# Kernel optimization log

Hardware: AMD Instinct MI355X
Metric: run time of the kernel (lower is better)

The kernel has to match this reference:

```python
import math
import jax, jax.numpy as jnp
import numpy as np

B = 64
INPUT_SIZE = 10080
PATCH = 18
S = INPUT_SIZE // PATCH  # 560 patches
E = 96                    # embed_dim
H = 12                    # num_heads
D = 96                    # head_dim == embed_dim (PAT quirk)
F = 256                   # ff_dim
L = 2                     # num_layers
EPS = 1e-5


def _sinusoidal_pe(seq_len, embed_dim):
    pos = jnp.arange(seq_len, dtype=jnp.float32)[:, None]
    div = jnp.exp(jnp.arange(0, embed_dim, 2, dtype=jnp.float32) * (-math.log(10000.0) / embed_dim))
    pe = jnp.zeros((seq_len, embed_dim), dtype=jnp.float32)
    pe = pe.at[:, 0::2].set(jnp.sin(pos * div))
    pe = pe.at[:, 1::2].set(jnp.cos(pos * div))
    return pe


def _layernorm(x, g, b):
    mu = jnp.mean(x, axis=-1, keepdims=True)
    var = jnp.var(x, axis=-1, keepdims=True)
    return (x - mu) * jax.lax.rsqrt(var + EPS) * g + b


def setup_inputs() -> dict:
    key = jax.random.key(0)
    ks = jax.random.split(key, 12)
    sd = 0.02
    inp = {
        "x": jax.random.normal(ks[0], (B, INPUT_SIZE), dtype=jnp.float32),
        "patch_W": jax.random.normal(ks[1], (PATCH, E), dtype=jnp.float32) * sd,
        "patch_b": jnp.zeros((E,), jnp.float32),
        "Wq": jax.random.normal(ks[2], (L, H, E, D), dtype=jnp.float32) * sd,
        "bq": jnp.zeros((L, H, D), jnp.float32),
        "Wk": jax.random.normal(ks[3], (L, H, E, D), dtype=jnp.float32) * sd,
        "bk": jnp.zeros((L, H, D), jnp.float32),
        "Wv": jax.random.normal(ks[4], (L, H, E, D), dtype=jnp.float32) * sd,
        "bv": jnp.zeros((L, H, D), jnp.float32),
        "Wo": jax.random.normal(ks[5], (L, H * D, E), dtype=jnp.float32) * sd,
        "bo": jnp.zeros((L, E), jnp.float32),
        "ff1_W": jax.random.normal(ks[6], (L, E, F), dtype=jnp.float32) * sd,
        "ff1_b": jnp.zeros((L, F), jnp.float32),
        "ff2_W": jax.random.normal(ks[7], (L, F, E), dtype=jnp.float32) * sd,
        "ff2_b": jnp.zeros((L, E), jnp.float32),
        "n1_g": jnp.ones((L, E), jnp.float32),
        "n1_b": jnp.zeros((L, E), jnp.float32),
        "n2_g": jnp.ones((L, E), jnp.float32),
        "n2_b": jnp.zeros((L, E), jnp.float32),
    }
    return inp


def reference(x, patch_W, patch_b, Wq, bq, Wk, bk, Wv, bv, Wo, bo,
              ff1_W, ff1_b, ff2_W, ff2_b, n1_g, n1_b, n2_g, n2_b):
    scale = 1.0 / math.sqrt(D)
    # patch embedding: [B, S, PATCH] -> [B, S, E]
    h = x.reshape(B, S, PATCH) @ patch_W + patch_b
    h = h + _sinusoidal_pe(S, E)[None]
    for l in range(L):
        # all heads at once (original loops over heads; same math)
        q = jnp.einsum('bse,hed->bhsd', h, Wq[l]) + bq[l][None, :, None, :]
        k = jnp.einsum('bse,hed->bhsd', h, Wk[l]) + bk[l][None, :, None, :]
        v = jnp.einsum('bse,hed->bhsd', h, Wv[l]) + bv[l][None, :, None, :]
        scores = jnp.einsum('bhsd,bhtd->bhst', q, k) * scale
        attn = jax.nn.softmax(scores, axis=-1)
        heads = jnp.einsum('bhst,bhtd->bhsd', attn, v)
        concat = heads.transpose(0, 2, 1, 3).reshape(B, S, H * D)
        attn_out = concat @ Wo[l] + bo[l]
        h = _layernorm(h + attn_out, n1_g[l], n1_b[l])
        ff = jax.nn.relu(h @ ff1_W[l] + ff1_b[l]) @ ff2_W[l] + ff2_b[l]
        h = _layernorm(h + ff, n2_g[l], n2_b[l])
    return h
```

## Files before the change

### kernel.cpp

```cpp
#include <hip/hip_runtime.h>
#include <hip/hip_bf16.h>
#include <math.h>

#define BATCH 64
#define CHUNK 32
#define INPUT_SIZE 10080
#define PATCH 18
#define SEQ 560
#define EMB 96
#define NHEAD 12
#define HDIM 96
#define FFDIM 256
#define NLAYER 2
#define TOK (BATCH * SEQ)
#define EPSV 1e-5f
#define SCALE 0.10206207261596577f
#define SCALE_L2E 0.14724443805513492f

typedef __attribute__((ext_vector_type(8))) short bf16x8;
typedef __attribute__((ext_vector_type(4))) short bf16x4;
typedef __attribute__((ext_vector_type(4))) float f32x4;
typedef __attribute__((ext_vector_type(2))) unsigned int u32x2;

static __device__ __forceinline__ short f2bf(float x) {
  union { __hip_bfloat16 b; short s; } u;
  u.b = __float2bfloat16(x);
  return u.s;
}

static __device__ __forceinline__ unsigned int pack2bf(float lo, float hi) {
  unsigned int a = (unsigned short)f2bf(lo);
  unsigned int b = (unsigned short)f2bf(hi);
  return a | (b << 16);
}

static __device__ __forceinline__ float exp2_fast(float x) {
  float r;
  asm("v_exp_f32 %0, %1" : "=v"(r) : "v"(x));
  return r;
}

__global__ __launch_bounds__(256) void allprep_kernel(
    const float* __restrict__ Wq, const float* __restrict__ Wk,
    const float* __restrict__ Wv, const float* __restrict__ Wo,
    const float* __restrict__ ff1_W, const float* __restrict__ ff2_W,
    __hip_bfloat16* __restrict__ wqT, __hip_bfloat16* __restrict__ wkvT,
    __hip_bfloat16* __restrict__ woT, __hip_bfloat16* __restrict__ ff1WT,
    __hip_bfloat16* __restrict__ ff2WT) {
  int bx = blockIdx.x;
  if (bx < 72) {
    int hh = bx % NHEAD, mat = (bx / NHEAD) % 3, l = bx / 36;
    const float* src = (mat == 0 ? Wq : (mat == 1 ? Wk : Wv)) +
                       ((size_t)l * NHEAD + hh) * EMB * HDIM;
    __shared__ float t[HDIM * 97];
    for (int i = threadIdx.x; i < EMB * HDIM; i += 256) {
      int e = i / HDIM, d = i % HDIM;
      t[d * 97 + e] = src[i];
    }
    __syncthreads();
    __hip_bfloat16* dst;
    if (mat == 0)
      dst = wqT + ((size_t)l * NHEAD + hh) * HDIM * EMB;
    else
      dst = wkvT + ((size_t)l * 2 * NHEAD * HDIM + (mat - 1) * NHEAD * HDIM +
                    hh * HDIM) * EMB;
    for (int j = threadIdx.x; j < HDIM * EMB; j += 256) {
      int d = j / EMB, e = j % EMB;
      dst[j] = __float2bfloat16(t[d * 97 + e]);
    }
  } else if (bx < 74) {
    int l = bx - 72;
    const float* src = Wo + (size_t)l * NHEAD * HDIM * EMB;
    __hip_bfloat16* dst = woT + (size_t)l * EMB * NHEAD * HDIM;
    for (int i = threadIdx.x; i < EMB * NHEAD * HDIM; i += 256) {
      int e = i / (NHEAD * HDIM), j = i % (NHEAD * HDIM);
      dst[i] = __float2bfloat16(src[(size_t)j * EMB + e]);
    }
  } else {
    int idx = bx - 74;
    int mat = idx % 2, l = idx / 2;
    if (mat == 0) {
      const float* src = ff1_W + (size_t)l * EMB * FFDIM;
      __hip_bfloat16* dst = ff1WT + (size_t)l * FFDIM * EMB;
      for (int i = threadIdx.x; i < FFDIM * EMB; i += 256) {
        int f = i / EMB, e = i % EMB;
        dst[i] = __float2bfloat16(src[(size_t)e * FFDIM + f]);
      }
    } else {
      const float* src = ff2_W + (size_t)l * FFDIM * EMB;
      __hip_bfloat16* dst = ff2WT + (size_t)l * EMB * FFDIM;
      for (int i = threadIdx.x; i < EMB * FFDIM; i += 256) {
        int e = i / FFDIM, f = i % FFDIM;
        dst[i] = __float2bfloat16(src[(size_t)f * EMB + e]);
      }
    }
  }
}

__global__ void patch_pe_kernel(const float* __restrict__ x,
                                const float* __restrict__ W,
                                const float* __restrict__ bias,
                                float* __restrict__ h,
                                __hip_bfloat16* __restrict__ hbf) {
  int gid = blockIdx.x * blockDim.x + threadIdx.x;
  if (gid >= TOK * EMB) return;
  int tok = gid / EMB;
  int e = gid % EMB;
  int b = tok / SEQ;
  int s = tok % SEQ;
  const float* xp = x + b * INPUT_SIZE + s * PATCH;
  float acc = bias[e];
#pragma unroll
  for (int p = 0; p < PATCH; p++) acc += xp[p] * W[p * EMB + e];
  int i = e >> 1;
  float freq = __expf(-(float)(2 * i) * (9.210340371976184f / 96.0f));
  float ang = (float)s * freq;
  acc += (e & 1) ? cosf(ang) : sinf(ang);
  h[gid] = acc;
  hbf[gid] = __float2bfloat16(acc);
}

__global__ __launch_bounds__(256) void kv_mfma_kernel(
    const __hip_bfloat16* __restrict__ hbf,
    const __hip_bfloat16* __restrict__ wkvT, const float* __restrict__ bk,
    const float* __restrict__ bv, __hip_bfloat16* __restrict__ kbuf,
    __hip_bfloat16* __restrict__ vbufT, int b0) {
  const int wave = threadIdx.x >> 6;
  const int lane = threadIdx.x & 63;
  const int tq = lane & 15;
  const int quad = lane >> 4;
  const int m0 = blockIdx.x * 64 + wave * 16;
  const int n0 = blockIdx.y * 64;

  __shared__ short tile[4][16][68];

  const short* ap =
      (const short*)hbf + ((size_t)b0 * SEQ + m0 + tq) * EMB + quad * 8;
  bf16x8 a0 = *(const bf16x8*)(ap);
  bf16x8 a1 = *(const bf16x8*)(ap + 32);
  bf16x8 a2 = *(const bf16x8*)(ap + 64);

  f32x4 acc[4];
  const f32x4 zero4 = {0.f, 0.f, 0.f, 0.f};
#pragma unroll
  for (int nt = 0; nt < 4; nt++) acc[nt] = zero4;
#pragma unroll
  for (int nt = 0; nt < 4; nt++) {
    const short* bp =
        (const short*)wkvT + (size_t)(n0 + nt * 16 + tq) * EMB + quad * 8;
    bf16x8 b0f = *(const bf16x8*)(bp);
    bf16x8 b1f = *(const bf16x8*)(bp + 32);
    bf16x8 b2f = *(const bf16x8*)(bp + 64);
    acc[nt] = __builtin_amdgcn_mfma_f32_16x16x32_bf16(a0, b0f, acc[nt], 0, 0, 0);
    acc[nt] = __builtin_amdgcn_mfma_f32_16x16x32_bf16(a1, b1f, acc[nt], 0, 0, 0);
    acc[nt] = __builtin_amdgcn_mfma_f32_16x16x32_bf16(a2, b2f, acc[nt], 0, 0, 0);
  }

  const int tl0 = m0 + quad * 4;
  const int blb = tl0 / SEQ;
  const int ss0 = tl0 - blb * SEQ;

  if (n0 < NHEAD * HDIM) {
#pragma unroll
    for (int nt = 0; nt < 4; nt++) {
      int n = n0 + nt * 16 + tq;
      float bias = bk[n];
#pragma unroll
      for (int j = 0; j < 4; j++)
        tile[wave][quad * 4 + j][nt * 16 + tq] = f2bf(acc[nt][j] + bias);
    }
#pragma unroll
    for (int it = 0; it < 2; it++) {
      int idx = it * 64 + lane;
      int row = idx >> 3;
      int seg = idx & 7;
      int tl = m0 + row;
      int bb = tl / SEQ;
      int ss = tl - bb * SEQ;
      int r0s = n0 + seg * 8;
      int hh2 = r0s / HDIM;
      int d0 = r0s - hh2 * HDIM;
      bf16x8 v = *(const bf16x8*)&tile[wave][row][seg * 8];
      *(bf16x8*)((short*)kbuf +
                 ((size_t)(bb * NHEAD + hh2) * SEQ + ss) * HDIM + d0) = v;
    }
  } else {
#pragma unroll
    for (int nt = 0; nt < 4; nt++) {
      int n = n0 + nt * 16 + tq;
      int r = n - NHEAD * HDIM;
      int hh2 = r / HDIM;
      int d = r - hh2 * HDIM;
      float bias = bv[r];
      bf16x4 pack;
#pragma unroll
      for (int j = 0; j < 4; j++) pack[j] = f2bf(acc[nt][j] + bias);
      *(bf16x4*)((short*)vbufT +
                 ((size_t)(blb * NHEAD + hh2) * HDIM + d) * SEQ + ss0) = pack;
    }
  }
}

#define QW 104
#define PW32 36
__global__ __launch_bounds__(256, 3) void attn_flash_kernel(
    const __hip_bfloat16* __restrict__ hbf,
    const __hip_bfloat16* __restrict__ wqT, const float* __restrict__ bq,
    const __hip_bfloat16* __restrict__ kbuf,
    const __hip_bfloat16* __restrict__ vbufT,
    __hip_bfloat16* __restrict__ heads, int b0) {
  const int flat = blockIdx.x;
  const int xcd = flat & 7;
  const int slot = flat >> 3;
  const int g = (slot / 5) * 8 + xcd;
  const int qt = slot % 5;
  const int hh = g % NHEAD;
  const int bl = g / NHEAD;
  const int wave = threadIdx.x >> 6;
  const int lane = threadIdx.x & 63;
  const int tq = lane & 15;
  const int quad = lane >> 4;

  __shared__ __align__(16) short sbuf[4][3328];
  short* pw = sbuf[wave];
  unsigned int* pwA = (unsigned int*)pw;
  unsigned int* pwB = pwA + 16 * PW32;

  const size_t bh = (size_t)(bl * NHEAD + hh);
  const short* kb = (const short*)kbuf + bh * SEQ * HDIM;
  const short* vb = (const short*)vbufT + bh * HDIM * SEQ;

  const int q0 = qt * 128 + wave * 32;

  int qrA = q0 + tq;      if (qrA > SEQ - 1) qrA = SEQ - 1;
  int qrB = q0 + 16 + tq; if (qrB > SEQ - 1) qrB = SEQ - 1;
  const short* hpA =
      (const short*)hbf + ((size_t)(b0 + bl) * SEQ + qrA) * EMB + quad * 8;
  const short* hpB =
      (const short*)hbf + ((size_t)(b0 + bl) * SEQ + qrB) * EMB + quad * 8;
  bf16x8 haA0 = *(const bf16x8*)(hpA);
  bf16x8 haA1 = *(const bf16x8*)(hpA + 32);
  bf16x8 haA2 = *(const bf16x8*)(hpA + 64);
  bf16x8 haB0 = *(const bf16x8*)(hpB);
  bf16x8 haB1 = *(const bf16x8*)(hpB + 32);
  bf16x8 haB2 = *(const bf16x8*)(hpB + 64);
  const f32x4 zero4 = {0.f, 0.f, 0.f, 0.f};
  f32x4 qaccA[6], qaccB[6];
#pragma unroll
  for (int dt = 0; dt < 6; dt++) { qaccA[dt] = zero4; qaccB[dt] = zero4; }
#pragma unroll
  for (int dt = 0; dt < 6; dt++) {
    const short* wp = (const short*)wqT +
                      ((size_t)hh * HDIM + dt * 16 + tq) * EMB + quad * 8;
    bf16x8 w0 = *(const bf16x8*)(wp);
    bf16x8 w1 = *(const bf16x8*)(wp + 32);
    bf16x8 w2 = *(const bf16x8*)(wp + 64);
    qaccA[dt] = __builtin_amdgcn_mfma_f32_16x16x32_bf16(haA0, w0, qaccA[dt], 0, 0, 0);
    qaccA[dt] = __builtin_amdgcn_mfma_f32_16x16x32_bf16(haA1, w1, qaccA[dt], 0, 0, 0);
    qaccA[dt] = __builtin_amdgcn_mfma_f32_16x16x32_bf16(haA2, w2, qaccA[dt], 0, 0, 0);
    qaccB[dt] = __builtin_amdgcn_mfma_f32_16x16x32_bf16(haB0, w0, qaccB[dt], 0, 0, 0);
    qaccB[dt] = __builtin_amdgcn_mfma_f32_16x16x32_bf16(haB1, w1, qaccB[dt], 0, 0, 0);
    qaccB[dt] = __builtin_amdgcn_mfma_f32_16x16x32_bf16(haB2, w2, qaccB[dt], 0, 0, 0);
  }
#pragma unroll
  for (int dt = 0; dt < 6; dt++) {
    int d = dt * 16 + tq;
    float bias = bq[hh * HDIM + d];
#pragma unroll
    for (int r = 0; r < 4; r++) {
      pw[(quad * 4 + r) * QW + d] = f2bf((qaccA[dt][r] + bias) * SCALE_L2E);
      pw[(16 + quad * 4 + r) * QW + d] = f2bf((qaccB[dt][r] + bias) * SCALE_L2E);
    }
  }
  bf16x8 aqA0 = *(const bf16x8*)&pw[tq * QW + quad * 8];
  bf16x8 aqA1 = *(const bf16x8*)&pw[tq * QW + 32 + quad * 8];
  bf16x8 aqA2 = *(const bf16x8*)&pw[tq * QW + 64 + quad * 8];
  bf16x8 aqB0 = *(const bf16x8*)&pw[(16 + tq) * QW + quad * 8];
  bf16x8 aqB1 = *(const bf16x8*)&pw[(16 + tq) * QW + 32 + quad * 8];
  bf16x8 aqB2 = *(const bf16x8*)&pw[(16 + tq) * QW + 64 + quad * 8];

  f32x4 oA[6], oB[6];
#pragma unroll
  for (int dt = 0; dt < 6; dt++) { oA[dt] = zero4; oB[dt] = zero4; }
  float mA = -1e30f, mB = -1e30f, lA = 0.f, lB = 0.f;

  for (int c = 0; c < 9; c++) {
    const int col0 = c * 64;
    f32x4 sA[4], sB[4];
#pragma unroll
    for (int t = 0; t < 4; t++) { sA[t] = zero4; sB[t] = zero4; }
#pragma unroll
    for (int t = 0; t < 4; t++) {
      const short* kp = kb + (size_t)(col0 + t * 16 + tq) * HDIM + quad * 8;
      bf16x8 k0 = *(const bf16x8*)(kp);
      bf16x8 k1 = *(const bf16x8*)(kp + 32);
      bf16x8 k2 = *(const bf16x8*)(kp + 64);
      sA[t] = __builtin_amdgcn_mfma_f32_16x16x32_bf16(k0, aqA0, sA[t], 0, 0, 0);
      sA[t] = __builtin_amdgcn_mfma_f32_16x16x32_bf16(k1, aqA1, sA[t], 0, 0, 0);
      sA[t] = __builtin_amdgcn_mfma_f32_16x16x32_bf16(k2, aqA2, sA[t], 0, 0, 0);
      sB[t] = __builtin_amdgcn_mfma_f32_16x16x32_bf16(k0, aqB0, sB[t], 0, 0, 0);
      sB[t] = __builtin_amdgcn_mfma_f32_16x16x32_bf16(k1, aqB1, sB[t], 0, 0, 0);
      sB[t] = __builtin_amdgcn_mfma_f32_16x16x32_bf16(k2, aqB2, sB[t], 0, 0, 0);
    }
    if (c == 8) {
#pragma unroll
      for (int r = 0; r < 4; r++) { sA[3][r] = -1e30f; sB[3][r] = -1e30f; }
    }
    float cA = sA[0][0], cB = sB[0][0];
#pragma unroll
    for (int t = 0; t < 4; t++) {
#pragma unroll
      for (int r = 0; r < 4; r++) {
        cA = fmaxf(cA, sA[t][r]);
        cB = fmaxf(cB, sB[t][r]);
      }
    }
    cA = fmaxf(cA, __shfl_xor(cA, 16, 64));
    cA = fmaxf(cA, __shfl_xor(cA, 32, 64));
    cB = fmaxf(cB, __shfl_xor(cB, 16, 64));
    cB = fmaxf(cB, __shfl_xor(cB, 32, 64));
    if (__any((cA > mA) | (cB > mB))) {
      float mnA = fmaxf(mA, cA);
      float fA = exp2_fast(mA - mnA);
      mA = mnA; lA *= fA;
      float mnB = fmaxf(mB, cB);
      float fB = exp2_fast(mB - mnB);
      mB = mnB; lB *= fB;
#pragma unroll
      for (int dt = 0; dt < 6; dt++) {
#pragma unroll
        for (int r = 0; r < 4; r++) { oA[dt][r] *= fA; oB[dt][r] *= fB; }
      }
    }
#pragma unroll
    for (int t = 0; t < 4; t++) {
      float pA0 = exp2_fast(sA[t][0] - mA);
      float pA1 = exp2_fast(sA[t][1] - mA);
      float pA2 = exp2_fast(sA[t][2] - mA);
      float pA3 = exp2_fast(sA[t][3] - mA);
      lA += (pA0 + pA1) + (pA2 + pA3);
      u32x2 wA = {pack2bf(pA0, pA1), pack2bf(pA2, pA3)};
      *(u32x2*)&pwA[tq * PW32 + t * 8 + quad * 2] = wA;
      float pB0 = exp2_fast(sB[t][0] - mB);
      float pB1 = exp2_fast(sB[t][1] - mB);
      float pB2 = exp2_fast(sB[t][2] - mB);
      float pB3 = exp2_fast(sB[t][3] - mB);
      lB += (pB0 + pB1) + (pB2 + pB3);
      u32x2 wB = {pack2bf(pB0, pB1), pack2bf(pB2, pB3)};
      *(u32x2*)&pwB[tq * PW32 + t * 8 + quad * 2] = wB;
    }
    bf16x8 paA0 = *(const bf16x8*)&pwA[tq * PW32 + quad * 4];
    bf16x8 paA1 = *(const bf16x8*)&pwA[tq * PW32 + 16 + quad * 4];
    bf16x8 paB0 = *(const bf16x8*)&pwB[tq * PW32 + quad * 4];
    bf16x8 paB1 = *(const bf16x8*)&pwB[tq * PW32 + 16 + quad * 4];
#pragma unroll
    for (int dt = 0; dt < 6; dt++) {
      const short* vp = vb + (size_t)(dt * 16 + tq) * SEQ + col0 + quad * 8;
      bf16x8 v0 = *(const bf16x8*)(vp);
      bf16x8 v1 = *(const bf16x8*)(vp + 32);
      oA[dt] = __builtin_amdgcn_mfma_f32_16x16x32_bf16(v0, paA0, oA[dt], 0, 0, 0);
      oA[dt] = __builtin_amdgcn_mfma_f32_16x16x32_bf16(v1, paA1, oA[dt], 0, 0, 0);
      oB[dt] = __builtin_amdgcn_mfma_f32_16x16x32_bf16(v0, paB0, oB[dt], 0, 0, 0);
      oB[dt] = __builtin_amdgcn_mfma_f32_16x16x32_bf16(v1, paB1, oB[dt], 0, 0, 0);
    }
  }

  lA += __shfl_xor(lA, 16, 64);
  lA += __shfl_xor(lA, 32, 64);
  lB += __shfl_xor(lB, 16, 64);
  lB += __shfl_xor(lB, 32, 64);
  float rA = 1.f / lA, rB = 1.f / lB;
  short* hpout =
      (short*)heads + ((size_t)(b0 + bl) * SEQ) * (NHEAD * HDIM) + hh * HDIM;
  const int tokA = q0 + tq;
  const int tokB = q0 + 16 + tq;
#pragma unroll
  for (int dt = 0; dt < 6; dt++) {
    int d0 = dt * 16 + quad * 4;
    if (tokA < SEQ) {
      bf16x4 pk;
#pragma unroll
      for (int r = 0; r < 4; r++) pk[r] = f2bf(oA[dt][r] * rA);
      *(bf16x4*)(hpout + (size_t)tokA * (NHEAD * HDIM) + d0) = pk;
    }
    if (tokB < SEQ) {
      bf16x4 pk;
#pragma unroll
      for (int r = 0; r < 4; r++) pk[r] = f2bf(oB[dt][r] * rB);
      *(bf16x4*)(hpout + (size_t)tokB * (NHEAD * HDIM) + d0) = pk;
    }
  }
}

__global__ __launch_bounds__(256) void wo_ln_mfma_kernel(
    const __hip_bfloat16* __restrict__ heads,
    const __hip_bfloat16* __restrict__ woT, const float* __restrict__ bo,
    const float* __restrict__ gamma, const float* __restrict__ beta,
    const float* __restrict__ hres, float* __restrict__ hA,
    __hip_bfloat16* __restrict__ hbf) {
  const int wave = threadIdx.x >> 6;
  const int lane = threadIdx.x & 63;
  const int tq = lane & 15;
  const int quad = lane >> 4;
  const int m0 = blockIdx.x * 64 + wave * 16;

  const short* ap = (const short*)heads + (size_t)(m0 + tq) * (NHEAD * HDIM);
  const short* bp = (const short*)woT;

  f32x4 acc[6];
  const f32x4 zero4 = {0.f, 0.f, 0.f, 0.f};
#pragma unroll
  for (int dt = 0; dt < 6; dt++) acc[dt] = zero4;

  for (int kt = 0; kt < 36; kt++) {
    bf16x8 af = *(const bf16x8*)(ap + kt * 32 + quad * 8);
#pragma unroll
    for (int dt = 0; dt < 6; dt++) {
      bf16x8 bfr = *(const bf16x8*)(bp + (size_t)(dt * 16 + tq) * (NHEAD * HDIM) +
                                    kt * 32 + quad * 8);
      acc[dt] = __builtin_amdgcn_mfma_f32_16x16x32_bf16(af, bfr, acc[dt], 0, 0, 0);
    }
  }

  const int tok0 = m0 + quad * 4;
  float s1[4] = {0.f, 0.f, 0.f, 0.f};
  float s2[4] = {0.f, 0.f, 0.f, 0.f};
#pragma unroll
  for (int dt = 0; dt < 6; dt++) {
    int n = dt * 16 + tq;
    float bias = bo[n];
#pragma unroll
    for (int r = 0; r < 4; r++) {
      float val = acc[dt][r] + bias + hres[(size_t)(tok0 + r) * EMB + n];
      acc[dt][r] = val;
      s1[r] += val;
      s2[r] += val * val;
    }
  }
#pragma unroll
  for (int mask = 1; mask < 16; mask <<= 1) {
#pragma unroll
    for (int r = 0; r < 4; r++) {
      s1[r] += __shfl_xor(s1[r], mask, 64);
      s2[r] += __shfl_xor(s2[r], mask, 64);
    }
  }
  float mean[4], rstd[4];
#pragma unroll
  for (int r = 0; r < 4; r++) {
    mean[r] = s1[r] * (1.0f / EMB);
    float var = s2[r] * (1.0f / EMB) - mean[r] * mean[r];
    rstd[r] = rsqrtf(var + EPSV);
  }
#pragma unroll
  for (int dt = 0; dt < 6; dt++) {
    int n = dt * 16 + tq;
    float g = gamma[n], bt = beta[n];
#pragma unroll
    for (int r = 0; r < 4; r++) {
      float o = (acc[dt][r] - mean[r]) * rstd[r] * g + bt;
      hA[(size_t)(tok0 + r) * EMB + n] = o;
      hbf[(size_t)(tok0 + r) * EMB + n] = __float2bfloat16(o);
    }
  }
}

__global__ __launch_bounds__(256) void ff1_mfma_kernel(
    const __hip_bfloat16* __restrict__ hbf,
    const __hip_bfloat16* __restrict__ ff1WT, const float* __restrict__ b1,
    __hip_bfloat16* __restrict__ ffbf) {
  const int wave = threadIdx.x >> 6;
  const int lane = threadIdx.x & 63;
  const int tq = lane & 15;
  const int quad = lane >> 4;
  const int m0 = blockIdx.x * 64 + wave * 16;

  const short* ap = (const short*)hbf + (size_t)(m0 + tq) * EMB + quad * 8;
  bf16x8 a0 = *(const bf16x8*)(ap);
  bf16x8 a1 = *(const bf16x8*)(ap + 32);
  bf16x8 a2 = *(const bf16x8*)(ap + 64);

  f32x4 acc[16];
  const f32x4 zero4 = {0.f, 0.f, 0.f, 0.f};
#pragma unroll
  for (int nt = 0; nt < 16; nt++) acc[nt] = zero4;
#pragma unroll
  for (int nt = 0; nt < 16; nt++) {
    const short* bp =
        (const short*)ff1WT + (size_t)(nt * 16 + tq) * EMB + quad * 8;
    bf16x8 b0f = *(const bf16x8*)(bp);
    bf16x8 b1f = *(const bf16x8*)(bp + 32);
    bf16x8 b2f = *(const bf16x8*)(bp + 64);
    acc[nt] = __builtin_amdgcn_mfma_f32_16x16x32_bf16(a0, b0f, acc[nt], 0, 0, 0);
    acc[nt] = __builtin_amdgcn_mfma_f32_16x16x32_bf16(a1, b1f, acc[nt], 0, 0, 0);
    acc[nt] = __builtin_amdgcn_mfma_f32_16x16x32_bf16(a2, b2f, acc[nt], 0, 0, 0);
  }

  const int tok0 = m0 + quad * 4;
#pragma unroll
  for (int nt = 0; nt < 16; nt++) {
    int n = nt * 16 + tq;
    float bias = b1[n];
#pragma unroll
    for (int r = 0; r < 4; r++) {
      ffbf[(size_t)(tok0 + r) * FFDIM + n] =
          __float2bfloat16(fmaxf(acc[nt][r] + bias, 0.f));
    }
  }
}

__global__ __launch_bounds__(256) void ff2_ln_mfma_kernel(
    const __hip_bfloat16* __restrict__ ffbf,
    const __hip_bfloat16* __restrict__ ff2WT, const float* __restrict__ b2,
    const float* __restrict__ gamma, const float* __restrict__ beta,
    const float* __restrict__ hres, float* __restrict__ hout,
    __hip_bfloat16* __restrict__ hbf_out) {
  const int wave = threadIdx.x >> 6;
  const int lane = threadIdx.x & 63;
  const int tq = lane & 15;
  const int quad = lane >> 4;
  const int m0 = blockIdx.x * 64 + wave * 16;

  const short* ap = (const short*)ffbf + (size_t)(m0 + tq) * FFDIM;
  const short* bp = (const short*)ff2WT;

  f32x4 acc[6];
  const f32x4 zero4 = {0.f, 0.f, 0.f, 0.f};
#pragma unroll
  for (int dt = 0; dt < 6; dt++) acc[dt] = zero4;

#pragma unroll
  for (int kt = 0; kt < 8; kt++) {
    bf16x8 af = *(const bf16x8*)(ap + kt * 32 + quad * 8);
#pragma unroll
    for (int dt = 0; dt < 6; dt++) {
      bf16x8 bfr = *(const bf16x8*)(bp + (size_t)(dt * 16 + tq) * FFDIM +
                                    kt * 32 + quad * 8);
      acc[dt] = __builtin_amdgcn_mfma_f32_16x16x32_bf16(af, bfr, acc[dt], 0, 0, 0);
    }
  }

  const int tok0 = m0 + quad * 4;
  float s1[4] = {0.f, 0.f, 0.f, 0.f};
  float s2[4] = {0.f, 0.f, 0.f, 0.f};
#pragma unroll
  for (int dt = 0; dt < 6; dt++) {
    int n = dt * 16 + tq;
    float bias = b2[n];
#pragma unroll
    for (int r = 0; r < 4; r++) {
      float val = acc[dt][r] + bias + hres[(size_t)(tok0 + r) * EMB + n];
      acc[dt][r] = val;
      s1[r] += val;
      s2[r] += val * val;
    }
  }
#pragma unroll
  for (int mask = 1; mask < 16; mask <<= 1) {
#pragma unroll
    for (int r = 0; r < 4; r++) {
      s1[r] += __shfl_xor(s1[r], mask, 64);
      s2[r] += __shfl_xor(s2[r], mask, 64);
    }
  }
  float mean[4], rstd[4];
#pragma unroll
  for (int r = 0; r < 4; r++) {
    mean[r] = s1[r] * (1.0f / EMB);
    float var = s2[r] * (1.0f / EMB) - mean[r] * mean[r];
    rstd[r] = rsqrtf(var + EPSV);
  }
#pragma unroll
  for (int dt = 0; dt < 6; dt++) {
    int n = dt * 16 + tq;
    float g = gamma[n], bt = beta[n];
#pragma unroll
    for (int r = 0; r < 4; r++) {
      float o = (acc[dt][r] - mean[r]) * rstd[r] * g + bt;
      hout[(size_t)(tok0 + r) * EMB + n] = o;
      hbf_out[(size_t)(tok0 + r) * EMB + n] = __float2bfloat16(o);
    }
  }
}

extern "C" void kernel_launch(void* const* d_in, const int* in_sizes, int n_in,
                              void* d_out, int out_size, void* d_ws,
                              size_t ws_size, hipStream_t stream) {
  const float* x = (const float*)d_in[0];
  const float* patch_W = (const float*)d_in[1];
  const float* patch_b = (const float*)d_in[2];
  const float* Wq = (const float*)d_in[3];
  const float* bq = (const float*)d_in[4];
  const float* Wk = (const float*)d_in[5];
  const float* bk = (const float*)d_in[6];
  const float* Wv = (const float*)d_in[7];
  const float* bv = (const float*)d_in[8];
  const float* Wo = (const float*)d_in[9];
  const float* bo = (const float*)d_in[10];
  const float* ff1_W = (const float*)d_in[11];
  const float* ff1_b = (const float*)d_in[12];
  const float* ff2_W = (const float*)d_in[13];
  const float* ff2_b = (const float*)d_in[14];
  const float* n1_g = (const float*)d_in[15];
  const float* n1_b = (const float*)d_in[16];
  const float* n2_g = (const float*)d_in[17];
  const float* n2_b = (const float*)d_in[18];

  const size_t h_bytes = (size_t)TOK * EMB * sizeof(float);
  const size_t hbf_bytes = (size_t)TOK * EMB * 2;
  const size_t kv_bytes = (size_t)CHUNK * NHEAD * SEQ * HDIM * 2;
  const size_t heads_bytes = (size_t)TOK * NHEAD * HDIM * 2;
  const size_t wqT_bytes = (size_t)NLAYER * NHEAD * HDIM * EMB * 2;
  const size_t wkvT_bytes = 2 * wqT_bytes;
  const size_t woT_bytes = (size_t)NLAYER * EMB * NHEAD * HDIM * 2;
  const size_t ffw_bytes = (size_t)NLAYER * FFDIM * EMB * 2;
  char* ws = (char*)d_ws;
  size_t off = 0;
  float* h = (float*)(ws + off); off += h_bytes;
  float* hA = (float*)(ws + off); off += h_bytes;
  __hip_bfloat16* hbf = (__hip_bfloat16*)(ws + off); off += hbf_bytes;
  __hip_bfloat16* kbuf = (__hip_bfloat16*)(ws + off); off += kv_bytes;
  __hip_bfloat16* vbufT = (__hip_bfloat16*)(ws + off); off += kv_bytes;
  __hip_bfloat16* heads = (__hip_bfloat16*)(ws + off); off += heads_bytes;
  __hip_bfloat16* wqT = (__hip_bfloat16*)(ws + off); off += wqT_bytes;
  __hip_bfloat16* wkvT = (__hip_bfloat16*)(ws + off); off += wkvT_bytes;
  __hip_bfloat16* woT = (__hip_bfloat16*)(ws + off); off += woT_bytes;
  __hip_bfloat16* ff1WT = (__hip_bfloat16*)(ws + off); off += ffw_bytes;
  __hip_bfloat16* ff2WT = (__hip_bfloat16*)(ws + off); off += ffw_bytes;
  __hip_bfloat16* ffbf = (__hip_bfloat16*)kbuf;

  allprep_kernel<<<78, 256, 0, stream>>>(Wq, Wk, Wv, Wo, ff1_W, ff2_W, wqT,
                                         wkvT, woT, ff1WT, ff2WT);
  patch_pe_kernel<<<(TOK * EMB + 255) / 256, 256, 0, stream>>>(x, patch_W,
                                                               patch_b, h, hbf);

  for (int l = 0; l < NLAYER; l++) {
    const __hip_bfloat16* wqT_l = wqT + (size_t)l * NHEAD * HDIM * EMB;
    const __hip_bfloat16* wkvT_l = wkvT + (size_t)l * 2 * NHEAD * HDIM * EMB;
    const __hip_bfloat16* woT_l = woT + (size_t)l * EMB * NHEAD * HDIM;
    const __hip_bfloat16* ff1WT_l = ff1WT + (size_t)l * FFDIM * EMB;
    const __hip_bfloat16* ff2WT_l = ff2WT + (size_t)l * EMB * FFDIM;
    const float* bq_l = bq + (size_t)l * NHEAD * HDIM;
    const float* bk_l = bk + (size_t)l * NHEAD * HDIM;
    const float* bv_l = bv + (size_t)l * NHEAD * HDIM;
    const float* bo_l = bo + (size_t)l * EMB;

    for (int c = 0; c < BATCH / CHUNK; c++) {
      int b0 = c * CHUNK;
      kv_mfma_kernel<<<dim3(CHUNK * SEQ / 64, 2 * NHEAD * HDIM / 64), 256, 0,
                       stream>>>(hbf, wkvT_l, bk_l, bv_l, kbuf, vbufT, b0);
      attn_flash_kernel<<<5 * NHEAD * CHUNK, 256, 0, stream>>>(
          hbf, wqT_l, bq_l, kbuf, vbufT, heads, b0);
    }
    wo_ln_mfma_kernel<<<TOK / 64, 256, 0, stream>>>(
        heads, woT_l, bo_l, n1_g + l * EMB, n1_b + l * EMB, h, hA, hbf);
    ff1_mfma_kernel<<<TOK / 64, 256, 0, stream>>>(hbf, ff1WT_l,
                                                  ff1_b + l * FFDIM, ffbf);
    float* dst = (l == NLAYER - 1) ? (float*)d_out : h;
    ff2_ln_mfma_kernel<<<TOK / 64, 256, 0, stream>>>(
        ffbf, ff2WT_l, ff2_b + l * EMB, n2_g + l * EMB, n2_b + l * EMB, hA,
        dst, hbf);
  }
}
```

Before: 1.193 ms.

## Split attention query tile across eight waves of sixteen rows each

The flash attention kernel now launches 512 threads per block, and each of the 8 waves handles 16 query rows instead of 32. Waves whose rows start past the sequence end exit early, which replaces the old clamping and per-row store guards. This halves per-wave accumulator registers and LDS to allow more resident waves per CU. In exchange, each K/V tile is now loaded by twice as many waves, so global/L2 traffic per query rises.

After: 1.462 ms. +22.6%, slower.

```diff
diff --git a/kernel.cpp b/kernel.cpp
--- a/kernel.cpp
+++ b/kernel.cpp
@@ -203,7 +203,7 @@
 
 #define QW 104
 #define PW32 36
-__global__ __launch_bounds__(256, 3) void attn_flash_kernel(
+__global__ __launch_bounds__(512, 4) void attn_flash_kernel(
     const __hip_bfloat16* __restrict__ hbf,
     const __hip_bfloat16* __restrict__ wqT, const float* __restrict__ bq,
     const __hip_bfloat16* __restrict__ kbuf,
@@ -221,33 +221,27 @@
   const int tq = lane & 15;
   const int quad = lane >> 4;
 
-  __shared__ __align__(16) short sbuf[4][3328];
+  __shared__ __align__(16) short sbuf[8][1664];
   short* pw = sbuf[wave];
   unsigned int* pwA = (unsigned int*)pw;
-  unsigned int* pwB = pwA + 16 * PW32;
+
+  const int q0 = qt * 128 + wave * 16;
+  if (q0 >= SEQ) return;
 
   const size_t bh = (size_t)(bl * NHEAD + hh);
   const short* kb = (const short*)kbuf + bh * SEQ * HDIM;
   const short* vb = (const short*)vbufT + bh * HDIM * SEQ;
 
-  const int q0 = qt * 128 + wave * 32;
-
-  int qrA = q0 + tq;      if (qrA > SEQ - 1) qrA = SEQ - 1;
-  int qrB = q0 + 16 + tq; if (qrB > SEQ - 1) qrB = SEQ - 1;
-  const short* hpA =
-      (const short*)hbf + ((size_t)(b0 + bl) * SEQ + qrA) * EMB + quad * 8;
-  const short* hpB =
-      (const short*)hbf + ((size_t)(b0 + bl) * SEQ + qrB) * EMB + quad * 8;
-  bf16x8 haA0 = *(const bf16x8*)(hpA);
-  bf16x8 haA1 = *(const bf16x8*)(hpA + 32);
-  bf16x8 haA2 = *(const bf16x8*)(hpA + 64);
-  bf16x8 haB0 = *(const bf16x8*)(hpB);
-  bf16x8 haB1 = *(const bf16x8*)(hpB + 32);
-  bf16x8 haB2 = *(const bf16x8*)(hpB + 64);
+  const int qr = q0 + tq;
+  const short* hp =
+      (const short*)hbf + ((size_t)(b0 + bl) * SEQ + qr) * EMB + quad * 8;
+  bf16x8 ha0 = *(const bf16x8*)(hp);
+  bf16x8 ha1 = *(const bf16x8*)(hp + 32);
+  bf16x8 ha2 = *(const bf16x8*)(hp + 64);
   const f32x4 zero4 = {0.f, 0.f, 0.f, 0.f};
-  f32x4 qaccA[6], qaccB[6];
-#pragma unroll
-  for (int dt = 0; dt < 6; dt++) { qaccA[dt] = zero4; qaccB[dt] = zero4; }
+  f32x4 qacc[6];
+#pragma unroll
+  for (int dt = 0; dt < 6; dt++) qacc[dt] = zero4;
 #pragma unroll
   for (int dt = 0; dt < 6; dt++) {
     const short* wp = (const short*)wqT +
@@ -255,140 +249,98 @@
     bf16x8 w0 = *(const bf16x8*)(wp);
     bf16x8 w1 = *(const bf16x8*)(wp + 32);
     bf16x8 w2 = *(const bf16x8*)(wp + 64);
-    qaccA[dt] = __builtin_amdgcn_mfma_f32_16x16x32_bf16(haA0, w0, qaccA[dt], 0, 0, 0);
-    qaccA[dt] = __builtin_amdgcn_mfma_f32_16x16x32_bf16(haA1, w1, qaccA[dt], 0, 0, 0);
-    qaccA[dt] = __builtin_amdgcn_mfma_f32_16x16x32_bf16(haA2, w2, qaccA[dt], 0, 0, 0);
-    qaccB[dt] = __builtin_amdgcn_mfma_f32_16x16x32_bf16(haB0, w0, qaccB[dt], 0, 0, 0);
-    qaccB[dt] = __builtin_amdgcn_mfma_f32_16x16x32_bf16(haB1, w1, qaccB[dt], 0, 0, 0);
-    qaccB[dt] = __builtin_amdgcn_mfma_f32_16x16x32_bf16(haB2, w2, qaccB[dt], 0, 0, 0);
+    qacc[dt] = __builtin_amdgcn_mfma_f32_16x16x32_bf16(ha0, w0, qacc[dt], 0, 0, 0);
+    qacc[dt] = __builtin_amdgcn_mfma_f32_16x16x32_bf16(ha1, w1, qacc[dt], 0, 0, 0);
+    qacc[dt] = __builtin_amdgcn_mfma_f32_16x16x32_bf16(ha2, w2, qacc[dt], 0, 0, 0);
   }
 #pragma unroll
   for (int dt = 0; dt < 6; dt++) {
     int d = dt * 16 + tq;
     float bias = bq[hh * HDIM + d];
 #pragma unroll
-    for (int r = 0; r < 4; r++) {
-      pw[(quad * 4 + r) * QW + d] = f2bf((qaccA[dt][r] + bias) * SCALE_L2E);
-      pw[(16 + quad * 4 + r) * QW + d] = f2bf((qaccB[dt][r] + bias) * SCALE_L2E);
-    }
-  }
-  bf16x8 aqA0 = *(const bf16x8*)&pw[tq * QW + quad * 8];
-  bf16x8 aqA1 = *(const bf16x8*)&pw[tq * QW + 32 + quad * 8];
-  bf16x8 aqA2 = *(const bf16x8*)&pw[tq * QW + 64 + quad * 8];
-  bf16x8 aqB0 = *(const bf16x8*)&pw[(16 + tq) * QW + quad * 8];
-  bf16x8 aqB1 = *(const bf16x8*)&pw[(16 + tq) * QW + 32 + quad * 8];
-  bf16x8 aqB2 = *(const bf16x8*)&pw[(16 + tq) * QW + 64 + quad * 8];
-
-  f32x4 oA[6], oB[6];
-#pragma unroll
-  for (int dt = 0; dt < 6; dt++) { oA[dt] = zero4; oB[dt] = zero4; }
-  float mA = -1e30f, mB = -1e30f, lA = 0.f, lB = 0.f;
+    for (int r = 0; r < 4; r++)
+      pw[(quad * 4 + r) * QW + d] = f2bf((qacc[dt][r] + bias) * SCALE_L2E);
+  }
+  bf16x8 aq0 = *(const bf16x8*)&pw[tq * QW + quad * 8];
+  bf16x8 aq1 = *(const bf16x8*)&pw[tq * QW + 32 + quad * 8];
+  bf16x8 aq2 = *(const bf16x8*)&pw[tq * QW + 64 + quad * 8];
+
+  f32x4 o[6];
+#pragma unroll
+  for (int dt = 0; dt < 6; dt++) o[dt] = zero4;
+  float m = -1e30f, l = 0.f;
 
   for (int c = 0; c < 9; c++) {
     const int col0 = c * 64;
-    f32x4 sA[4], sB[4];
-#pragma unroll
-    for (int t = 0; t < 4; t++) { sA[t] = zero4; sB[t] = zero4; }
+    f32x4 s[4];
+#pragma unroll
+    for (int t = 0; t < 4; t++) s[t] = zero4;
 #pragma unroll
     for (int t = 0; t < 4; t++) {
       const short* kp = kb + (size_t)(col0 + t * 16 + tq) * HDIM + quad * 8;
       bf16x8 k0 = *(const bf16x8*)(kp);
       bf16x8 k1 = *(const bf16x8*)(kp + 32);
       bf16x8 k2 = *(const bf16x8*)(kp + 64);
-      sA[t] = __builtin_amdgcn_mfma_f32_16x16x32_bf16(k0, aqA0, sA[t], 0, 0, 0);
-      sA[t] = __builtin_amdgcn_mfma_f32_16x16x32_bf16(k1, aqA1, sA[t], 0, 0, 0);
-      sA[t] = __builtin_amdgcn_mfma_f32_16x16x32_bf16(k2, aqA2, sA[t], 0, 0, 0);
-      sB[t] = __builtin_amdgcn_mfma_f32_16x16x32_bf16(k0, aqB0, sB[t], 0, 0, 0);
-      sB[t] = __builtin_amdgcn_mfma_f32_16x16x32_bf16(k1, aqB1, sB[t], 0, 0, 0);
-      sB[t] = __builtin_amdgcn_mfma_f32_16x16x32_bf16(k2, aqB2, sB[t], 0, 0, 0);
+      s[t] = __builtin_amdgcn_mfma_f32_16x16x32_bf16(k0, aq0, s[t], 0, 0, 0);
+      s[t] = __builtin_amdgcn_mfma_f32_16x16x32_bf16(k1, aq1, s[t], 0, 0, 0);
+      s[t] = __builtin_amdgcn_mfma_f32_16x16x32_bf16(k2, aq2, s[t], 0, 0, 0);
     }
     if (c == 8) {
 #pragma unroll
-      for (int r = 0; r < 4; r++) { sA[3][r] = -1e30f; sB[3][r] = -1e30f; }
-    }
-    float cA = sA[0][0], cB = sB[0][0];
+      for (int r = 0; r < 4; r++) s[3][r] = -1e30f;
+    }
+    float cm = s[0][0];
 #pragma unroll
     for (int t = 0; t < 4; t++) {
 #pragma unroll
-      for (int r = 0; r < 4; r++) {
-        cA = fmaxf(cA, sA[t][r]);
-        cB = fmaxf(cB, sB[t][r]);
+      for (int r = 0; r < 4; r++) cm = fmaxf(cm, s[t][r]);
+    }
+    cm = fmaxf(cm, __shfl_xor(cm, 16, 64));
+    cm = fmaxf(cm, __shfl_xor(cm, 32, 64));
+    if (__any(cm > m)) {
+      float mn = fmaxf(m, cm);
+      float f = exp2_fast(m - mn);
+      m = mn; l *= f;
+#pragma unroll
+      for (int dt = 0; dt < 6; dt++) {
+#pragma unroll
+        for (int r = 0; r < 4; r++) o[dt][r] *= f;
       }
     }
-    cA = fmaxf(cA, __shfl_xor(cA, 16, 64));
-    cA = fmaxf(cA, __shfl_xor(cA, 32, 64));
-    cB = fmaxf(cB, __shfl_xor(cB, 16, 64));
-    cB = fmaxf(cB, __shfl_xor(cB, 32, 64));
-    if (__any((cA > mA) | (cB > mB))) {
-      float mnA = fmaxf(mA, cA);
-      float fA = exp2_fast(mA - mnA);
-      mA = mnA; lA *= fA;
-      float mnB = fmaxf(mB, cB);
-      float fB = exp2_fast(mB - mnB);
-      mB = mnB; lB *= fB;
-#pragma unroll
-      for (int dt = 0; dt < 6; dt++) {
-#pragma unroll
-        for (int r = 0; r < 4; r++) { oA[dt][r] *= fA; oB[dt][r] *= fB; }
-      }
-    }
 #pragma unroll
     for (int t = 0; t < 4; t++) {
-      float pA0 = exp2_fast(sA[t][0] - mA);
-      float pA1 = exp2_fast(sA[t][1] - mA);
-      float pA2 = exp2_fast(sA[t][2] - mA);
-      float pA3 = exp2_fast(sA[t][3] - mA);
-      lA += (pA0 + pA1) + (pA2 + pA3);
-      u32x2 wA = {pack2bf(pA0, pA1), pack2bf(pA2, pA3)};
-      *(u32x2*)&pwA[tq * PW32 + t * 8 + quad * 2] = wA;
-      float pB0 = exp2_fast(sB[t][0] - mB);
-      float pB1 = exp2_fast(sB[t][1] - mB);
-      float pB2 = exp2_fast(sB[t][2] - mB);
-      float pB3 = exp2_fast(sB[t][3] - mB);
-      lB += (pB0 + pB1) + (pB2 + pB3);
-      u32x2 wB = {pack2bf(pB0, pB1), pack2bf(pB2, pB3)};
-      *(u32x2*)&pwB[tq * PW32 + t * 8 + quad * 2] = wB;
-    }
-    bf16x8 paA0 = *(const bf16x8*)&pwA[tq * PW32 + quad * 4];
-    bf16x8 paA1 = *(const bf16x8*)&pwA[tq * PW32 + 16 + quad * 4];
-    bf16x8 paB0 = *(const bf16x8*)&pwB[tq * PW32 + quad * 4];
-    bf16x8 paB1 = *(const bf16x8*)&pwB[tq * PW32 + 16 + quad * 4];
+      float p0 = exp2_fast(s[t][0] - m);
+      float p1 = exp2_fast(s[t][1] - m);
+      float p2 = exp2_fast(s[t][2] - m);
+      float p3 = exp2_fast(s[t][3] - m);
+      l += (p0 + p1) + (p2 + p3);
+      u32x2 w = {pack2bf(p0, p1), pack2bf(p2, p3)};
+      *(u32x2*)&pwA[tq * PW32 + t * 8 + quad * 2] = w;
+    }
+    bf16x8 pa0 = *(const bf16x8*)&pwA[tq * PW32 + quad * 4];
+    bf16x8 pa1 = *(const bf16x8*)&pwA[tq * PW32 + 16 + quad * 4];
 #pragma unroll
     for (int dt = 0; dt < 6; dt++) {
       const short* vp = vb + (size_t)(dt * 16 + tq) * SEQ + col0 + quad * 8;
       bf16x8 v0 = *(const bf16x8*)(vp);
       bf16x8 v1 = *(const bf16x8*)(vp + 32);
-      oA[dt] = __builtin_amdgcn_mfma_f32_16x16x32_bf16(v0, paA0, oA[dt], 0, 0, 0);
-      oA[dt] = __builtin_amdgcn_mfma_f32_16x16x32_bf16(v1, paA1, oA[dt], 0, 0, 0);
-      oB[dt] = __builtin_amdgcn_mfma_f32_16x16x32_bf16(v0, paB0, oB[dt], 0, 0, 0);
-      oB[dt] = __builtin_amdgcn_mfma_f32_16x16x32_bf16(v1, paB1, oB[dt], 0, 0, 0);
-    }
-  }
-
-  lA += __shfl_xor(lA, 16, 64);
-  lA += __shfl_xor(lA, 32, 64);
-  lB += __shfl_xor(lB, 16, 64);
-  lB += __shfl_xor(lB, 32, 64);
-  float rA = 1.f / lA, rB = 1.f / lB;
-  short* hpout =
-      (short*)heads + ((size_t)(b0 + bl) * SEQ) * (NHEAD * HDIM) + hh * HDIM;
-  const int tokA = q0 + tq;
-  const int tokB = q0 + 16 + tq;
+      o[dt] = __builtin_amdgcn_mfma_f32_16x16x32_bf16(v0, pa0, o[dt], 0, 0, 0);
+      o[dt] = __builtin_amdgcn_mfma_f32_16x16x32_bf16(v1, pa1, o[dt], 0, 0, 0);
+    }
+  }
+
+  l += __shfl_xor(l, 16, 64);
+  l += __shfl_xor(l, 32, 64);
+  float rcp = 1.f / l;
+  short* hpout = (short*)heads +
+                 ((size_t)(b0 + bl) * SEQ + q0 + tq) * (NHEAD * HDIM) +
+                 hh * HDIM;
 #pragma unroll
   for (int dt = 0; dt < 6; dt++) {
-    int d0 = dt * 16 + quad * 4;
-    if (tokA < SEQ) {
-      bf16x4 pk;
-#pragma unroll
-      for (int r = 0; r < 4; r++) pk[r] = f2bf(oA[dt][r] * rA);
-      *(bf16x4*)(hpout + (size_t)tokA * (NHEAD * HDIM) + d0) = pk;
-    }
-    if (tokB < SEQ) {
-      bf16x4 pk;
-#pragma unroll
-      for (int r = 0; r < 4; r++) pk[r] = f2bf(oB[dt][r] * rB);
-      *(bf16x4*)(hpout + (size_t)tokB * (NHEAD * HDIM) + d0) = pk;
-    }
+    bf16x4 pk;
+#pragma unroll
+    for (int r = 0; r < 4; r++) pk[r] = f2bf(o[dt][r] * rcp);
+    *(bf16x4*)(hpout + dt * 16 + quad * 4) = pk;
   }
 }
 
@@ -649,7 +601,7 @@
       int b0 = c * CHUNK;
       kv_mfma_kernel<<<dim3(CHUNK * SEQ / 64, 2 * NHEAD * HDIM / 64), 256, 0,
                        stream>>>(hbf, wkvT_l, bk_l, bv_l, kbuf, vbufT, b0);
-      attn_flash_kernel<<<5 * NHEAD * CHUNK, 256, 0, stream>>>(
+      attn_flash_kernel<<<5 * NHEAD * CHUNK, 512, 0, stream>>>(
           hbf, wqT_l, bq_l, kbuf, vbufT, heads, b0);
     }
     wo_ln_mfma_kernel<<<TOK / 64, 256, 0, stream>>>(
```
